# Kernel tuning notes

Hardware: AMD Instinct MI355X
Metric: run time of the kernel (lower is better)

The kernel has to match this reference:

```python
import jax, jax.numpy as jnp
import numpy as np

B, L, D, H = 8, 2048, 1024, 1024
BASE_LR, BASE_WD = 0.01, 0.9


def setup_inputs() -> dict:
    key = jax.random.key(0)
    ks = jax.random.split(key, 8)
    s = 1.0 / np.sqrt(D)
    return {
        "x": jax.random.normal(ks[0], (B, L, D), jnp.float32),
        "hidden": jax.random.normal(ks[1], (B, D, H), jnp.float32),
        "log_base_lr": jnp.array([np.log(BASE_LR)], jnp.float32),
        "w_lr": jax.random.normal(ks[2], (D, 1), jnp.float32) * s,
        "b_lr": jnp.zeros((1,), jnp.float32),
        "log_base_wd": jnp.array([np.log(BASE_WD)], jnp.float32),
        "w_wd": jax.random.normal(ks[3], (D, 1), jnp.float32) * s,
        "b_wd": jnp.zeros((1,), jnp.float32),
        "w_q": jax.random.normal(ks[4], (D, H), jnp.float32) * s,
        "b_q": jnp.zeros((H,), jnp.float32),
        "w_k": jax.random.normal(ks[5], (D, H), jnp.float32) * s,
        "b_k": jnp.zeros((H,), jnp.float32),
        "w_v": jax.random.normal(ks[6], (D, D), jnp.float32) * s,
        "b_v": jnp.zeros((D,), jnp.float32),
    }


def reference(x, hidden, log_base_lr, w_lr, b_lr, log_base_wd, w_wd, b_wd,
              w_q, b_q, w_k, b_k, w_v, b_v):
    batch, length, dim = x.shape
    W_prev = hidden  # [b, d, h]
    query = x @ w_q + b_q                     # [b, l, h]
    key = x @ w_k + b_k                       # [b, l, h]
    value = x @ w_v + b_v                     # [b, l, d]
    lr = jnp.exp(log_base_lr) * jax.nn.sigmoid((x @ w_lr + b_lr)[..., 0])  # [b, l]
    # log(1 - base_wd * sigmoid(.)) via log1p for stability; same math.
    log_wd = jnp.log1p(-jnp.exp(log_base_wd) * jax.nn.sigmoid((x @ w_wd + b_wd)[..., 0]))  # [b, l]
    wd_cross = jnp.exp(jnp.cumsum(log_wd, axis=1))  # [b, l]
    # inner-chunk decay: entry [b, m, l] = exp(sum_{j=m+1..l} log_wd[b, j]) for l >= m
    tri = jnp.triu(jnp.broadcast_to(log_wd[:, None, :], (batch, length, length)), k=1)
    wd_inner = jnp.triu(jnp.exp(jnp.cumsum(tri, axis=2)))  # [b, l, l]
    kq = jnp.einsum('bld,bmd->blm', key, query)            # [b, l, m]
    mask_kq = kq * wd_inner
    WpK_V = jnp.einsum('bdh,blh->bld', W_prev, key) - value  # [b, l, d]
    y_inner = -jnp.einsum('bld,bl,blm->bmd', WpK_V, lr, mask_kq)
    y_cross = jnp.einsum('bdh,blh,bl->bld', W_prev, query, wd_cross)
    y = y_inner + y_cross
    W_next_inner = -jnp.einsum('bld,bl,blh->bdh', WpK_V, lr * wd_inner[:, :, -1], key)
    W_next_cross = W_prev * wd_cross[:, -1][:, None, None]
    W_next = W_next_inner + W_next_cross
    return y, W_next
```

## Files before the change

kernel.cpp:

```cpp
#include <hip/hip_runtime.h>
#include <stdint.h>

#define BB 8
#define LL 2048
#define DD 1024
#define HH 1024
#define BL (BB*LL)

typedef __attribute__((ext_vector_type(8))) short short8;
typedef __attribute__((ext_vector_type(4))) float f32x4;

__device__ __forceinline__ unsigned short f2bf(float f) {
  unsigned int x = __float_as_uint(f);
  unsigned int r = (x + 0x7fffu + ((x >> 16) & 1u)) >> 16;
  return (unsigned short)r;
}
__device__ __forceinline__ float bf2f(unsigned short u) {
  return __uint_as_float(((unsigned int)u) << 16);
}

__device__ __forceinline__ void stage16(const unsigned short* g, unsigned short* l) {
  __builtin_amdgcn_global_load_lds((const __attribute__((address_space(1))) void*)g,
                                   (__attribute__((address_space(3))) void*)l,
                                   16, 0, 0);
}

template<int MI>
struct __align__(16) SmemT {
  unsigned short a[2][MI*2048];
  unsigned short b[2][16384];
};

template<int MI>
__device__ __forceinline__ void acc_initT(f32x4 (&acc)[MI][4]) {
#pragma unroll
  for (int i = 0; i < MI; ++i)
#pragma unroll
    for (int j = 0; j < 4; ++j)
      acc[i][j] = (f32x4){0.f, 0.f, 0.f, 0.f};
}

#define SCB __builtin_amdgcn_sched_barrier(0)
#define LGKM0 do { asm volatile("s_waitcnt lgkmcnt(0)" ::: "memory"); SCB; } while (0)

template<int MI, class FA, class FB>
__device__ __forceinline__ void gemm10_core(FA srcA, FB srcB, int NK,
                                            SmemT<MI>* sm, f32x4 (&acc)[MI][4]) {
  const int lane = threadIdx.x & 63;
  const int wave = threadIdx.x >> 6;
  const int srow = lane >> 3;
  const int scol = ((lane & 7) ^ srow) * 8;
  const int fk = (lane >> 4) * 8;
  const int fr = lane & 15;
  const int fx = fr & 7;
  const int mwr = (wave >> 2) * (MI * 16);
  const int nwr = (wave & 3) * 64;
  const int cA0 = (MI == 8) ? ((wave < 4) ? 2 * wave : 2 * wave + 8) : 2 * wave;
  const int cA1 = cA0 + 8;
  const int cB0 = (wave >> 1) * 8 + 2 * (wave & 1);
  const int cB1 = cB0 + 4;
  const int kc0 = (((fk >> 3) ^ fx) << 3);
  const int kc1 = ((((32 + fk) >> 3) ^ fx) << 3);

  auto SA2 = [&](int p, int kt, int c) {
    stage16(srcA(c * 8 + srow, kt) + scol, &sm->a[p][c * 512]);
    stage16(srcA(c * 8 + 8 + srow, kt) + scol, &sm->a[p][(c + 1) * 512]);
  };
  auto SB2 = [&](int p, int kt, int c) {
    stage16(srcB(c * 8 + srow, kt) + scol, &sm->b[p][c * 512]);
    stage16(srcB(c * 8 + 8 + srow, kt) + scol, &sm->b[p][(c + 1) * 512]);
  };

  short8 af[4], bfv[4][2];
  auto LDB = [&](int p) {
#pragma unroll
    for (int j = 0; j < 4; ++j) {
      bfv[j][0] = *(const short8*)&sm->b[p][(nwr + j * 16 + fr) * 64 + kc0];
      bfv[j][1] = *(const short8*)&sm->b[p][(nwr + j * 16 + fr) * 64 + kc1];
    }
  };
  auto LDA4 = [&](int p, int iho, int kc) {
#pragma unroll
    for (int i = 0; i < 4; ++i)
      af[i] = *(const short8*)&sm->a[p][(mwr + iho + i * 16 + fr) * 64 + kc];
  };
  auto MMk = [&](int accb, int kk) {
#pragma unroll
    for (int i = 0; i < 4; ++i)
#pragma unroll
      for (int j = 0; j < 4; ++j)
        acc[accb + i][j] = __builtin_amdgcn_mfma_f32_16x16x32_bf16(
            af[i], bfv[j][kk], acc[accb + i][j], 0, 0, 0);
  };

  SA2(0, 0, cA0);
  if constexpr (MI == 8) SA2(0, 0, cA1);
  SB2(0, 0, cB0); SB2(0, 0, cB1);
  if (NK > 1) {
    SB2(1, 1, cB0); SB2(1, 1, cB1);
    asm volatile("s_waitcnt vmcnt(4)" ::: "memory");
  } else {
    asm volatile("s_waitcnt vmcnt(0)" ::: "memory");
  }
  SCB; __builtin_amdgcn_s_barrier(); SCB;

  for (int t = 0; t < NK; ++t) {
    const int p = t & 1, po = p ^ 1;
    const bool s1 = (t + 1 < NK), s2 = (t + 2 < NK);
    if (s1) { SA2(po, t + 1, cA0); if constexpr (MI == 8) SA2(po, t + 1, cA1); }
    LDB(p);
    LDA4(p, 0, kc0);
    LGKM0;
    __builtin_amdgcn_s_setprio(1); MMk(0, 0); __builtin_amdgcn_s_setprio(0);
    if constexpr (MI == 8) {
      LDA4(p, 0, kc1);
      LGKM0;
      __builtin_amdgcn_s_setprio(1); MMk(0, 1); __builtin_amdgcn_s_setprio(0);
      SCB; __builtin_amdgcn_s_barrier(); SCB;
      if (s2) { SB2(p, t + 2, cB0); SB2(p, t + 2, cB1); }
      LDA4(p, 64, kc0);
      LGKM0;
      __builtin_amdgcn_s_setprio(1); MMk(4, 0); __builtin_amdgcn_s_setprio(0);
      LDA4(p, 64, kc1);
      LGKM0;
      __builtin_amdgcn_s_setprio(1); MMk(4, 1); __builtin_amdgcn_s_setprio(0);
    } else {
      SCB; __builtin_amdgcn_s_barrier(); SCB;
      if (s2) { SB2(p, t + 2, cB0); SB2(p, t + 2, cB1); }
      LDA4(p, 0, kc1);
      LGKM0;
      __builtin_amdgcn_s_setprio(1); MMk(0, 1); __builtin_amdgcn_s_setprio(0);
    }
    SCB;
    if (s2)      { asm volatile("s_waitcnt vmcnt(4)" ::: "memory"); }
    else if (s1) { asm volatile("s_waitcnt vmcnt(0)" ::: "memory"); }
    SCB; __builtin_amdgcn_s_barrier(); SCB;
  }
}

template<int MI, typename F>
__device__ __forceinline__ void epiT(const f32x4 (&acc)[MI][4], F body) {
  const int lane = threadIdx.x & 63;
  const int wave = threadIdx.x >> 6;
  const int mwr = (wave >> 2) * (MI * 16), nwr = (wave & 3) * 64;
#pragma unroll
  for (int i = 0; i < MI; ++i)
#pragma unroll
    for (int j = 0; j < 4; ++j)
#pragma unroll
      for (int jj = 0; jj < 4; ++jj)
        body(mwr + i * 16 + ((lane >> 4) << 2) + jj,
             nwr + j * 16 + (lane & 15), acc[i][j][jj]);
}


__global__ void k_prep_x(const float* __restrict__ x, const float* __restrict__ wlr,
                         const float* __restrict__ wwd, unsigned short* __restrict__ xb,
                         float* __restrict__ lrlog, float* __restrict__ wdlog) {
  const int wave = threadIdx.x >> 6, lane = threadIdx.x & 63;
  const int row = blockIdx.x * 4 + wave;
  const float* xr = x + (size_t)row * DD;
  float s1 = 0.f, s2 = 0.f;
#pragma unroll
  for (int ch = 0; ch < 4; ++ch) {
    const int col = ch * 256 + lane * 4;
    float4 v = *(const float4*)(xr + col);
    float4 a = *(const float4*)(wlr + col);
    float4 b = *(const float4*)(wwd + col);
    s1 += v.x*a.x + v.y*a.y + v.z*a.z + v.w*a.w;
    s2 += v.x*b.x + v.y*b.y + v.z*b.z + v.w*b.w;
    uint2 u;
    u.x = (unsigned)f2bf(v.x) | ((unsigned)f2bf(v.y) << 16);
    u.y = (unsigned)f2bf(v.z) | ((unsigned)f2bf(v.w) << 16);
    *(uint2*)(xb + (size_t)row * DD + col) = u;
  }
#pragma unroll
  for (int off = 32; off > 0; off >>= 1) {
    s1 += __shfl_down(s1, off);
    s2 += __shfl_down(s2, off);
  }
  if (lane == 0) { lrlog[row] = s1; wdlog[row] = s2; }
}

__global__ void k_prep_w(const float* __restrict__ wq, const float* __restrict__ wk,
                         const float* __restrict__ wv, unsigned short* __restrict__ wqt,
                         unsigned short* __restrict__ wkt, unsigned short* __restrict__ wvtn,
                         unsigned short* __restrict__ wkr) {
  const int idx = blockIdx.x * 256 + threadIdx.x;
  if (blockIdx.z == 3) { wkr[idx] = f2bf(wk[idx]); return; }
  const int k = idx >> 10, n = idx & 1023;
  const float* src = (blockIdx.z == 0) ? wq : (blockIdx.z == 1) ? wk : wv;
  unsigned short* dst = (blockIdx.z == 0) ? wqt : (blockIdx.z == 1) ? wkt : wvtn;
  float v = src[(size_t)k * 1024 + n];
  if (blockIdx.z == 2) v = -v;
  dst[(size_t)n * 1024 + k] = f2bf(v);
}

__global__ void k_prep_h(const float* __restrict__ hid, unsigned short* __restrict__ wpb) {
  const size_t i = ((size_t)blockIdx.x * 256 + threadIdx.x) * 4;
  float4 v = *(const float4*)(hid + i);
  uint2 u;
  u.x = (unsigned)f2bf(v.x) | ((unsigned)f2bf(v.y) << 16);
  u.y = (unsigned)f2bf(v.z) | ((unsigned)f2bf(v.w) << 16);
  *(uint2*)(wpb + i) = u;
}

__global__ void k_bias2(const unsigned short* __restrict__ wpb, const float* __restrict__ bk,
                        const float* __restrict__ bv, float* __restrict__ bias2) {
  const int wave = threadIdx.x >> 6, lane = threadIdx.x & 63;
  const int row = blockIdx.x * 4 + wave;
  const unsigned short* wr = wpb + (size_t)row * HH;
  float s = 0.f;
#pragma unroll
  for (int ch = 0; ch < 4; ++ch) {
    const int col = ch * 256 + lane * 4;
    float4 a = *(const float4*)(bk + col);
    ushort4 u = *(const ushort4*)(wr + col);
    s += a.x * bf2f(u.x) + a.y * bf2f(u.y) + a.z * bf2f(u.z) + a.w * bf2f(u.w);
  }
#pragma unroll
  for (int off = 32; off > 0; off >>= 1) s += __shfl_down(s, off);
  if (lane == 0) bias2[row] = s - bv[row & 1023];
}

__global__ void k_scan(const float* __restrict__ lrlog, const float* __restrict__ wdlog,
                       const float* __restrict__ lbl, const float* __restrict__ blr,
                       const float* __restrict__ lbw, const float* __restrict__ bwd,
                       float* __restrict__ lr, float* __restrict__ c,
                       float* __restrict__ s, float* __restrict__ ecl) {
  const int b = blockIdx.x, t = threadIdx.x;
  __shared__ float sums[256];
  const float elr = expf(lbl[0]);
  const float ewd = expf(lbw[0]);
  const float blr0 = blr[0], bwd0 = bwd[0];
  float lw[8];
  const float* wb = wdlog + (size_t)b * LL + t * 8;
  float tot = 0.f;
#pragma unroll
  for (int i = 0; i < 8; ++i) {
    float z = wb[i] + bwd0;
    float sig = 1.f / (1.f + expf(-z));
    tot += log1pf(-ewd * sig);
    lw[i] = tot;
  }
  sums[t] = tot;
  __syncthreads();
  for (int off = 1; off < 256; off <<= 1) {
    float v = (t >= off) ? sums[t - off] : 0.f;
    __syncthreads();
    sums[t] += v;
    __syncthreads();
  }
  const float prev = (t > 0) ? sums[t - 1] : 0.f;
  const float ctot = sums[255];
  const float* lb = lrlog + (size_t)b * LL + t * 8;
#pragma unroll
  for (int i = 0; i < 8; ++i) {
    const int idx = b * LL + t * 8 + i;
    const float ci = prev + lw[i];
    c[idx] = ci;
    float zl = lb[i] + blr0;
    float lri = elr / (1.f + expf(-zl));
    lr[idx] = lri;
    s[idx] = lri * expf(ctot - ci);
  }
  if (t == 0) ecl[b] = expf(ctot);
}


__global__ __launch_bounds__(512, 2) void k10_gemm_m2(const unsigned short* __restrict__ wpb,
    const unsigned short* __restrict__ wkr, const unsigned short* __restrict__ wvtn,
    unsigned short* __restrict__ w2t) {
  __shared__ SmemT<4> sm;
  const int b = blockIdx.x;
  const int mt = blockIdx.y & 7, nt = blockIdx.y >> 3;
  const int m0 = mt * 128, n0 = nt * 256;
  f32x4 acc[4][4]; acc_initT<4>(acc);
  gemm10_core<4>(
    [&](int r, int kt) { return wpb + (size_t)b * DD * HH + (size_t)(m0 + r) * HH + kt * 64; },
    [&](int r, int kt) { return wkr + (size_t)(n0 + r) * HH + kt * 64; },
    HH / 64, &sm, acc);
  epiT<4>(acc, [&](int rr, int cc, float av) {
    const size_t gi = (size_t)(m0 + rr) * DD + (n0 + cc);
    w2t[(size_t)b * DD * DD + gi] = f2bf(av + bf2f(wvtn[gi]));
  });
}

__global__ __launch_bounds__(512, 2) void k10_gemm_q(const unsigned short* __restrict__ xb,
    const unsigned short* __restrict__ wt, const float* __restrict__ bias,
    const float* __restrict__ c, unsigned short* __restrict__ outb,
    unsigned short* __restrict__ q2b) {
  __shared__ SmemT<8> sm;
  const int mt = blockIdx.x * 8 + (blockIdx.y & 7);
  const int nt = blockIdx.y >> 3;
  const int m0 = mt * 256, n0 = nt * 256;
  f32x4 acc[8][4]; acc_initT<8>(acc);
  gemm10_core<8>(
    [&](int r, int kt) { return xb + (size_t)(m0 + r) * DD + kt * 64; },
    [&](int r, int kt) { return wt + (size_t)(n0 + r) * DD + kt * 64; },
    DD / 64, &sm, acc);
  const int lane = threadIdx.x & 63, wave = threadIdx.x >> 6;
  const int mwr = (wave >> 2) * 128, nwr = (wave & 3) * 64;
  float er[8][4];
#pragma unroll
  for (int i = 0; i < 8; ++i)
#pragma unroll
    for (int jj = 0; jj < 4; ++jj)
      er[i][jj] = __expf(c[m0 + mwr + i * 16 + ((lane >> 4) << 2) + jj]);
#pragma unroll
  for (int i = 0; i < 8; ++i)
#pragma unroll
    for (int j = 0; j < 4; ++j)
#pragma unroll
      for (int jj = 0; jj < 4; ++jj) {
        const int row = m0 + mwr + i * 16 + ((lane >> 4) << 2) + jj;
        const int col = n0 + nwr + j * 16 + (lane & 15);
        const float v = acc[i][j][jj] + bias[col];
        outb[(size_t)row * HH + col] = f2bf(v);
        q2b[(size_t)row * HH + col] = f2bf(v * er[i][jj]);
      }
}

__global__ __launch_bounds__(512, 2) void k10_gemm_k(const unsigned short* __restrict__ xb,
    const unsigned short* __restrict__ wt, const float* __restrict__ bias,
    const float* __restrict__ s, unsigned short* __restrict__ kb,
    unsigned short* __restrict__ k2t) {
  __shared__ SmemT<8> sm;
  const int mt = blockIdx.x * 8 + (blockIdx.y & 7);
  const int nt = blockIdx.y >> 3;
  const int m0 = mt * 256, n0 = nt * 256;
  f32x4 acc[8][4]; acc_initT<8>(acc);
  gemm10_core<8>(
    [&](int r, int kt) { return xb + (size_t)(m0 + r) * DD + kt * 64; },
    [&](int r, int kt) { return wt + (size_t)(n0 + r) * DD + kt * 64; },
    DD / 64, &sm, acc);
  const int lane = threadIdx.x & 63, wave = threadIdx.x >> 6;
  const int mwr = (wave >> 2) * 128, nwr = (wave & 3) * 64;
#pragma unroll
  for (int i = 0; i < 8; ++i)
#pragma unroll
    for (int j = 0; j < 4; ++j) {
      const int col = n0 + nwr + j * 16 + (lane & 15);
      const float bias_c = bias[col];
      const int row0 = m0 + mwr + i * 16 + ((lane >> 4) << 2);
      const int b = row0 >> 11, ml0 = row0 & 2047;
      unsigned short tmp[4];
#pragma unroll
      for (int jj = 0; jj < 4; ++jj) {
        float v = acc[i][j][jj] + bias_c;
        kb[(size_t)(row0 + jj) * HH + col] = f2bf(v);
        tmp[jj] = f2bf(v * s[row0 + jj]);
      }
      uint2 u;
      u.x = (unsigned)tmp[0] | ((unsigned)tmp[1] << 16);
      u.y = (unsigned)tmp[2] | ((unsigned)tmp[3] << 16);
      *(uint2*)&k2t[((size_t)b * HH + col) * LL + ml0] = u;
    }
}

__global__ __launch_bounds__(512, 2) void k10_gemm_u(const unsigned short* __restrict__ xb,
    const unsigned short* __restrict__ w2t, const float* __restrict__ bias2,
    unsigned short* __restrict__ ut) {
  __shared__ SmemT<8> sm;
  const int b = blockIdx.x;
  const int mt = blockIdx.x * 8 + (blockIdx.y & 7);
  const int nt = blockIdx.y >> 3;
  const int m0 = mt * 256, n0 = nt * 256;
  f32x4 acc[8][4]; acc_initT<8>(acc);
  gemm10_core<8>(
    [&](int r, int kt) { return xb + (size_t)(m0 + r) * DD + kt * 64; },
    [&](int r, int kt) { return w2t + (size_t)b * DD * DD + (size_t)(n0 + r) * DD + kt * 64; },
    DD / 64, &sm, acc);
  const int lane = threadIdx.x & 63, wave = threadIdx.x >> 6;
  const int mwr = (wave >> 2) * 128, nwr = (wave & 3) * 64;
#pragma unroll
  for (int i = 0; i < 8; ++i)
#pragma unroll
    for (int j = 0; j < 4; ++j) {
      const int col = n0 + nwr + j * 16 + (lane & 15);
      const float b2c = bias2[b * DD + col];
      const int row0 = m0 + mwr + i * 16 + ((lane >> 4) << 2);
      const int ml0 = row0 & 2047;
      unsigned short tmp[4];
#pragma unroll
      for (int jj = 0; jj < 4; ++jj) tmp[jj] = f2bf(acc[i][j][jj] + b2c);
      uint2 u;
      u.x = (unsigned)tmp[0] | ((unsigned)tmp[1] << 16);
      u.y = (unsigned)tmp[2] | ((unsigned)tmp[3] << 16);
      *(uint2*)&ut[((size_t)b * DD + col) * LL + ml0] = u;
    }
}

__global__ __launch_bounds__(512, 2) void k10_gemm_p(const unsigned short* __restrict__ qb,
    const unsigned short* __restrict__ kb, const float* __restrict__ lr,
    const float* __restrict__ c, unsigned short* __restrict__ pb) {
  __shared__ SmemT<4> sm;
  const int b = blockIdx.x;
  const int t = blockIdx.y;
  int r = (int)((sqrtf(4.f * (float)t + 1.f) - 1.f) * 0.5f);
  while ((r + 1) * (r + 2) <= t) ++r;
  while (r * (r + 1) > t) --r;
  const int u = t - r * (r + 1);
  const int mt = 2 * r + (u > r ? 1 : 0);
  const int nt2 = (u > r) ? (u - r - 1) : u;
  const int base = b * LL;
  const int m0 = mt * 128, n0 = nt2 * 256;
  f32x4 acc[4][4]; acc_initT<4>(acc);
  gemm10_core<4>(
    [&](int rr, int kt) { return qb + (size_t)(base + m0 + rr) * HH + kt * 64; },
    [&](int rr, int kt) { return kb + (size_t)(base + n0 + rr) * HH + kt * 64; },
    HH / 64, &sm, acc);
  epiT<4>(acc, [&](int rr, int cc, float av) {
    const int m = m0 + rr, l = n0 + cc;
    float v = 0.f;
    if (l <= m) v = -av * lr[base + l] * __expf(c[base + m] - c[base + l]);
    pb[((size_t)base + m) * LL + l] = f2bf(v);
  });
}

__global__ __launch_bounds__(512, 2) void k10_gemm_y(const unsigned short* __restrict__ pb,
    const unsigned short* __restrict__ ut, const unsigned short* __restrict__ q2b,
    const unsigned short* __restrict__ wpb, float* __restrict__ out) {
  __shared__ SmemT<4> sm;
  const int b = blockIdx.x;
  const int sr = blockIdx.y & 7, nt = blockIdx.y >> 3;
  const int n0 = nt * 256;
  const unsigned short* pbB = pb + (size_t)b * LL * LL;
  const unsigned short* utB = ut + (size_t)b * DD * LL;
  const unsigned short* q2B = q2b + (size_t)b * LL * HH;
  const unsigned short* wpB = wpb + (size_t)b * DD * HH;
  f32x4 acc[4][4];
#pragma unroll
  for (int job = 0; job < 2; ++job) {
    const int mt = job ? (15 - sr) : sr;
    const int m0 = mt * 128;
    const int NK1 = (mt + 1) * 2;
    acc_initT<4>(acc);
    gemm10_core<4>(
      [&](int r, int kt) {
        return (kt < NK1) ? pbB + (size_t)(m0 + r) * LL + kt * 64
                          : q2B + (size_t)(m0 + r) * HH + (kt - NK1) * 64;
      },
      [&](int r, int kt) {
        return (kt < NK1) ? utB + (size_t)(n0 + r) * LL + kt * 64
                          : wpB + (size_t)(n0 + r) * HH + (kt - NK1) * 64;
      },
      NK1 + 16, &sm, acc);
    epiT<4>(acc, [&](int rr, int cc, float av) {
      out[((size_t)b * LL + m0 + rr) * DD + (n0 + cc)] = av;
    });
  }
}

__global__ __launch_bounds__(512, 2) void k10_gemm_wn(const unsigned short* __restrict__ ut,
    const unsigned short* __restrict__ k2t, const float* __restrict__ hid,
    const float* __restrict__ ecl, float* __restrict__ out2) {
  __shared__ SmemT<4> sm;
  const int b = blockIdx.x;
  const int mt = blockIdx.y & 7, nt = blockIdx.y >> 3;
  const int m0 = mt * 128, n0 = nt * 256;
  f32x4 acc[4][4]; acc_initT<4>(acc);
  gemm10_core<4>(
    [&](int r, int kt) { return ut + (size_t)b * DD * LL + (size_t)(m0 + r) * LL + kt * 64; },
    [&](int r, int kt) { return k2t + (size_t)b * HH * LL + (size_t)(n0 + r) * LL + kt * 64; },
    LL / 64, &sm, acc);
  const float eclb = ecl[b];
  epiT<4>(acc, [&](int rr, int cc, float av) {
    const size_t gi = ((size_t)b * DD + (m0 + rr)) * HH + (n0 + cc);
    out2[gi] = -av + eclb * hid[gi];
  });
}


extern "C" void kernel_launch(void* const* d_in, const int* in_sizes, int n_in,
                              void* d_out, int out_size, void* d_ws, size_t ws_size,
                              hipStream_t stream) {
  (void)in_sizes; (void)n_in; (void)out_size; (void)ws_size;
  const float* x   = (const float*)d_in[0];
  const float* hid = (const float*)d_in[1];
  const float* lbl = (const float*)d_in[2];
  const float* wlr = (const float*)d_in[3];
  const float* blr = (const float*)d_in[4];
  const float* lbw = (const float*)d_in[5];
  const float* wwd = (const float*)d_in[6];
  const float* bwd = (const float*)d_in[7];
  const float* wq  = (const float*)d_in[8];
  const float* bq  = (const float*)d_in[9];
  const float* wk  = (const float*)d_in[10];
  const float* bk  = (const float*)d_in[11];
  const float* wv  = (const float*)d_in[12];
  const float* bv  = (const float*)d_in[13];
  float* out = (float*)d_out;

  char* w = (char*)d_ws;
  constexpr size_t SZ_XB  = (size_t)BL * DD * 2;
  constexpr size_t SZ_QB  = (size_t)BL * HH * 2;
  constexpr size_t SZ_KB  = (size_t)BL * HH * 2;
  constexpr size_t SZ_K2T = (size_t)BB * HH * LL * 2;
  constexpr size_t SZ_UT  = (size_t)BB * DD * LL * 2;
  constexpr size_t SZ_PB  = (size_t)BB * LL * LL * 2;
  constexpr size_t SZ_WT  = (size_t)DD * HH * 2;
  constexpr size_t SZ_WPB = (size_t)BB * DD * HH * 2;
  constexpr size_t SZ_V16 = (size_t)BL * 4;

  size_t off = 0;
  unsigned short* xb   = (unsigned short*)(w + off); off += SZ_XB;
  unsigned short* qb   = (unsigned short*)(w + off); off += SZ_QB;
  unsigned short* kb   = (unsigned short*)(w + off); off += SZ_KB;
  unsigned short* k2t  = (unsigned short*)(w + off); off += SZ_K2T;
  unsigned short* ut   = (unsigned short*)(w + off); off += SZ_UT;
  unsigned short* pb   = (unsigned short*)(w + off); off += SZ_PB;
  unsigned short* wqt  = (unsigned short*)(w + off); off += SZ_WT;
  unsigned short* wkt  = (unsigned short*)(w + off); off += SZ_WT;
  unsigned short* wvtn = (unsigned short*)(w + off); off += SZ_WT;
  unsigned short* wpb  = (unsigned short*)(w + off); off += SZ_WPB;
  float* lrlog = (float*)(w + off); off += SZ_V16;
  float* wdlog = (float*)(w + off); off += SZ_V16;
  float* lr    = (float*)(w + off); off += SZ_V16;
  float* c     = (float*)(w + off); off += SZ_V16;
  float* s     = (float*)(w + off); off += SZ_V16;
  float* ecl   = (float*)(w + off); off += 256;
  float* bias2 = (float*)(w + off); off += (size_t)BB * DD * 4;

  unsigned short* w2t = pb;
  unsigned short* wkr = pb + (size_t)BB * DD * DD;

  unsigned short* q2b = (unsigned short*)(out + (size_t)BL * DD);
  float* out2 = out + (size_t)BL * DD;

  k_prep_x<<<dim3(BL / 4), 256, 0, stream>>>(x, wlr, wwd, xb, lrlog, wdlog);
  k_prep_w<<<dim3(4096, 1, 4), 256, 0, stream>>>(wq, wk, wv, wqt, wkt, wvtn, wkr);
  k_prep_h<<<dim3((unsigned)((size_t)BB * DD * HH / 1024)), 256, 0, stream>>>(hid, wpb);
  k_scan<<<dim3(BB), 256, 0, stream>>>(lrlog, wdlog, lbl, blr, lbw, bwd, lr, c, s, ecl);
  k_bias2<<<dim3(BB * DD / 4), 256, 0, stream>>>(wpb, bk, bv, bias2);

  k10_gemm_m2<<<dim3(8, 32), 512, 0, stream>>>(wpb, wkr, wvtn, w2t);
  k10_gemm_q<<<dim3(8, 32), 512, 0, stream>>>(xb, wqt, bq, c, qb, q2b);
  k10_gemm_k<<<dim3(8, 32), 512, 0, stream>>>(xb, wkt, bk, s, kb, k2t);
  k10_gemm_u<<<dim3(8, 32), 512, 0, stream>>>(xb, w2t, bias2, ut);
  k10_gemm_p<<<dim3(8, 72), 512, 0, stream>>>(qb, kb, lr, c, pb);
  k10_gemm_y<<<dim3(8, 32), 512, 0, stream>>>(pb, ut, q2b, wpb, out);
  k10_gemm_wn<<<dim3(8, 32), 512, 0, stream>>>(ut, k2t, hid, ecl, out2);
}
```

Baseline: 581.2 us.

## Split MI=8 GEMM k-step into barrier-separated phases and retile y GEMM to 256 rows

In the 256-row GEMM core, each k-step is split into four phases. Each phase loads its own B and A fragments and issues part of the next tile's global-to-LDS staging, then runs a workgroup barrier before its MFMAs, so memory traffic spreads across the step and waves stay in lockstep. Separately, the y GEMM drops its 128-row, two-job triangular balancing in favour of one 256-row tile per block using the MI=8 core. That gives more reuse per tile but risks load imbalance, because row tiles now have different causal K lengths and the pairing no longer evens them out. The extra barriers per k-step may also add stalls.

```diff
diff --git a/kernel.cpp b/kernel.cpp
--- a/kernel.cpp
+++ b/kernel.cpp
@@ -44,7 +44,7 @@
 #define LGKM0 do { asm volatile("s_waitcnt lgkmcnt(0)" ::: "memory"); SCB; } while (0)
 
 template<int MI, class FA, class FB>
-__device__ __forceinline__ void gemm10_core(FA srcA, FB srcB, int NK,
+__device__ __forceinline__ void gemm11_core(FA srcA, FB srcB, int NK,
                                             SmemT<MI>* sm, f32x4 (&acc)[MI][4]) {
   const int lane = threadIdx.x & 63;
   const int wave = threadIdx.x >> 6;
@@ -79,6 +79,11 @@
       bfv[j][1] = *(const short8*)&sm->b[p][(nwr + j * 16 + fr) * 64 + kc1];
     }
   };
+  auto LDBk = [&](int p, int kk, int kc) {
+#pragma unroll
+    for (int j = 0; j < 4; ++j)
+      bfv[j][kk] = *(const short8*)&sm->b[p][(nwr + j * 16 + fr) * 64 + kc];
+  };
   auto LDA4 = [&](int p, int iho, int kc) {
 #pragma unroll
     for (int i = 0; i < 4; ++i)
@@ -107,34 +112,48 @@
   for (int t = 0; t < NK; ++t) {
     const int p = t & 1, po = p ^ 1;
     const bool s1 = (t + 1 < NK), s2 = (t + 2 < NK);
-    if (s1) { SA2(po, t + 1, cA0); if constexpr (MI == 8) SA2(po, t + 1, cA1); }
-    LDB(p);
-    LDA4(p, 0, kc0);
-    LGKM0;
-    __builtin_amdgcn_s_setprio(1); MMk(0, 0); __builtin_amdgcn_s_setprio(0);
     if constexpr (MI == 8) {
+      LDBk(p, 0, kc0);
+      LDA4(p, 0, kc0);
+      if (s1) SA2(po, t + 1, cA0);
+      SCB; __builtin_amdgcn_s_barrier(); LGKM0;
+      __builtin_amdgcn_s_setprio(1); MMk(0, 0); __builtin_amdgcn_s_setprio(0);
+      SCB; __builtin_amdgcn_s_barrier(); SCB;
+      LDBk(p, 1, kc1);
       LDA4(p, 0, kc1);
-      LGKM0;
+      if (s1) SA2(po, t + 1, cA1);
+      SCB; __builtin_amdgcn_s_barrier(); LGKM0;
       __builtin_amdgcn_s_setprio(1); MMk(0, 1); __builtin_amdgcn_s_setprio(0);
       SCB; __builtin_amdgcn_s_barrier(); SCB;
-      if (s2) { SB2(p, t + 2, cB0); SB2(p, t + 2, cB1); }
       LDA4(p, 64, kc0);
+      if (s2) SB2(p, t + 2, cB0);
+      SCB; __builtin_amdgcn_s_barrier(); LGKM0;
+      __builtin_amdgcn_s_setprio(1); MMk(4, 0); __builtin_amdgcn_s_setprio(0);
+      SCB; __builtin_amdgcn_s_barrier(); SCB;
+      LDA4(p, 64, kc1);
+      if (s2) SB2(p, t + 2, cB1);
+      SCB; __builtin_amdgcn_s_barrier(); LGKM0;
+      __builtin_amdgcn_s_setprio(1); MMk(4, 1); __builtin_amdgcn_s_setprio(0);
+      SCB;
+      if (s2)      { asm volatile("s_waitcnt vmcnt(4)" ::: "memory"); }
+      else if (s1) { asm volatile("s_waitcnt vmcnt(0)" ::: "memory"); }
+      SCB; __builtin_amdgcn_s_barrier(); SCB;
+    } else {
+      if (s1) SA2(po, t + 1, cA0);
+      LDB(p);
+      LDA4(p, 0, kc0);
       LGKM0;
-      __builtin_amdgcn_s_setprio(1); MMk(4, 0); __builtin_amdgcn_s_setprio(0);
-      LDA4(p, 64, kc1);
-      LGKM0;
-      __builtin_amdgcn_s_setprio(1); MMk(4, 1); __builtin_amdgcn_s_setprio(0);
-    } else {
+      __builtin_amdgcn_s_setprio(1); MMk(0, 0); __builtin_amdgcn_s_setprio(0);
       SCB; __builtin_amdgcn_s_barrier(); SCB;
       if (s2) { SB2(p, t + 2, cB0); SB2(p, t + 2, cB1); }
       LDA4(p, 0, kc1);
       LGKM0;
       __builtin_amdgcn_s_setprio(1); MMk(0, 1); __builtin_amdgcn_s_setprio(0);
+      SCB;
+      if (s2)      { asm volatile("s_waitcnt vmcnt(4)" ::: "memory"); }
+      else if (s1) { asm volatile("s_waitcnt vmcnt(0)" ::: "memory"); }
+      SCB; __builtin_amdgcn_s_barrier(); SCB;
     }
-    SCB;
-    if (s2)      { asm volatile("s_waitcnt vmcnt(4)" ::: "memory"); }
-    else if (s1) { asm volatile("s_waitcnt vmcnt(0)" ::: "memory"); }
-    SCB; __builtin_amdgcn_s_barrier(); SCB;
   }
 }
 
@@ -268,7 +287,7 @@
 }
 
 
-__global__ __launch_bounds__(512, 2) void k10_gemm_m2(const unsigned short* __restrict__ wpb,
+__global__ __launch_bounds__(512, 2) void k11_gemm_m2(const unsigned short* __restrict__ wpb,
     const unsigned short* __restrict__ wkr, const unsigned short* __restrict__ wvtn,
     unsigned short* __restrict__ w2t) {
   __shared__ SmemT<4> sm;
@@ -276,7 +295,7 @@
   const int mt = blockIdx.y & 7, nt = blockIdx.y >> 3;
   const int m0 = mt * 128, n0 = nt * 256;
   f32x4 acc[4][4]; acc_initT<4>(acc);
-  gemm10_core<4>(
+  gemm11_core<4>(
     [&](int r, int kt) { return wpb + (size_t)b * DD * HH + (size_t)(m0 + r) * HH + kt * 64; },
     [&](int r, int kt) { return wkr + (size_t)(n0 + r) * HH + kt * 64; },
     HH / 64, &sm, acc);
@@ -286,7 +305,7 @@
   });
 }
 
-__global__ __launch_bounds__(512, 2) void k10_gemm_q(const unsigned short* __restrict__ xb,
+__global__ __launch_bounds__(512, 2) void k11_gemm_q(const unsigned short* __restrict__ xb,
     const unsigned short* __restrict__ wt, const float* __restrict__ bias,
     const float* __restrict__ c, unsigned short* __restrict__ outb,
     unsigned short* __restrict__ q2b) {
@@ -295,7 +314,7 @@
   const int nt = blockIdx.y >> 3;
   const int m0 = mt * 256, n0 = nt * 256;
   f32x4 acc[8][4]; acc_initT<8>(acc);
-  gemm10_core<8>(
+  gemm11_core<8>(
     [&](int r, int kt) { return xb + (size_t)(m0 + r) * DD + kt * 64; },
     [&](int r, int kt) { return wt + (size_t)(n0 + r) * DD + kt * 64; },
     DD / 64, &sm, acc);
@@ -321,7 +340,7 @@
       }
 }
 
-__global__ __launch_bounds__(512, 2) void k10_gemm_k(const unsigned short* __restrict__ xb,
+__global__ __launch_bounds__(512, 2) void k11_gemm_k(const unsigned short* __restrict__ xb,
     const unsigned short* __restrict__ wt, const float* __restrict__ bias,
     const float* __restrict__ s, unsigned short* __restrict__ kb,
     unsigned short* __restrict__ k2t) {
@@ -330,7 +349,7 @@
   const int nt = blockIdx.y >> 3;
   const int m0 = mt * 256, n0 = nt * 256;
   f32x4 acc[8][4]; acc_initT<8>(acc);
-  gemm10_core<8>(
+  gemm11_core<8>(
     [&](int r, int kt) { return xb + (size_t)(m0 + r) * DD + kt * 64; },
     [&](int r, int kt) { return wt + (size_t)(n0 + r) * DD + kt * 64; },
     DD / 64, &sm, acc);
@@ -358,7 +377,7 @@
     }
 }
 
-__global__ __launch_bounds__(512, 2) void k10_gemm_u(const unsigned short* __restrict__ xb,
+__global__ __launch_bounds__(512, 2) void k11_gemm_u(const unsigned short* __restrict__ xb,
     const unsigned short* __restrict__ w2t, const float* __restrict__ bias2,
     unsigned short* __restrict__ ut) {
   __shared__ SmemT<8> sm;
@@ -367,7 +386,7 @@
   const int nt = blockIdx.y >> 3;
   const int m0 = mt * 256, n0 = nt * 256;
   f32x4 acc[8][4]; acc_initT<8>(acc);
-  gemm10_core<8>(
+  gemm11_core<8>(
     [&](int r, int kt) { return xb + (size_t)(m0 + r) * DD + kt * 64; },
     [&](int r, int kt) { return w2t + (size_t)b * DD * DD + (size_t)(n0 + r) * DD + kt * 64; },
     DD / 64, &sm, acc);
@@ -391,7 +410,7 @@
     }
 }
 
-__global__ __launch_bounds__(512, 2) void k10_gemm_p(const unsigned short* __restrict__ qb,
+__global__ __launch_bounds__(512, 2) void k11_gemm_p(const unsigned short* __restrict__ qb,
     const unsigned short* __restrict__ kb, const float* __restrict__ lr,
     const float* __restrict__ c, unsigned short* __restrict__ pb) {
   __shared__ SmemT<4> sm;
@@ -406,7 +425,7 @@
   const int base = b * LL;
   const int m0 = mt * 128, n0 = nt2 * 256;
   f32x4 acc[4][4]; acc_initT<4>(acc);
-  gemm10_core<4>(
+  gemm11_core<4>(
     [&](int rr, int kt) { return qb + (size_t)(base + m0 + rr) * HH + kt * 64; },
     [&](int rr, int kt) { return kb + (size_t)(base + n0 + rr) * HH + kt * 64; },
     HH / 64, &sm, acc);
@@ -418,41 +437,32 @@
   });
 }
 
-__global__ __launch_bounds__(512, 2) void k10_gemm_y(const unsigned short* __restrict__ pb,
+__global__ __launch_bounds__(512, 2) void k11_gemm_y(const unsigned short* __restrict__ pb,
     const unsigned short* __restrict__ ut, const unsigned short* __restrict__ q2b,
     const unsigned short* __restrict__ wpb, float* __restrict__ out) {
-  __shared__ SmemT<4> sm;
+  __shared__ SmemT<8> sm;
   const int b = blockIdx.x;
-  const int sr = blockIdx.y & 7, nt = blockIdx.y >> 3;
-  const int n0 = nt * 256;
-  const unsigned short* pbB = pb + (size_t)b * LL * LL;
-  const unsigned short* utB = ut + (size_t)b * DD * LL;
-  const unsigned short* q2B = q2b + (size_t)b * LL * HH;
-  const unsigned short* wpB = wpb + (size_t)b * DD * HH;
-  f32x4 acc[4][4];
-#pragma unroll
-  for (int job = 0; job < 2; ++job) {
-    const int mt = job ? (15 - sr) : sr;
-    const int m0 = mt * 128;
-    const int NK1 = (mt + 1) * 2;
-    acc_initT<4>(acc);
-    gemm10_core<4>(
-      [&](int r, int kt) {
-        return (kt < NK1) ? pbB + (size_t)(m0 + r) * LL + kt * 64
-                          : q2B + (size_t)(m0 + r) * HH + (kt - NK1) * 64;
-      },
-      [&](int r, int kt) {
-        return (kt < NK1) ? utB + (size_t)(n0 + r) * LL + kt * 64
-                          : wpB + (size_t)(n0 + r) * HH + (kt - NK1) * 64;
-      },
-      NK1 + 16, &sm, acc);
-    epiT<4>(acc, [&](int rr, int cc, float av) {
-      out[((size_t)b * LL + m0 + rr) * DD + (n0 + cc)] = av;
-    });
-  }
-}
-
-__global__ __launch_bounds__(512, 2) void k10_gemm_wn(const unsigned short* __restrict__ ut,
+  const int mt = blockIdx.y & 7;
+  const int nt = blockIdx.y >> 3;
+  const int m0 = mt * 256, n0 = nt * 256;
+  const int NK1 = (mt + 1) * 4;
+  f32x4 acc[8][4]; acc_initT<8>(acc);
+  gemm11_core<8>(
+    [&](int r, int kt) {
+      return (kt < NK1) ? pb + (size_t)b * LL * LL + (size_t)(m0 + r) * LL + kt * 64
+                        : q2b + ((size_t)b * LL + m0 + r) * HH + (kt - NK1) * 64;
+    },
+    [&](int r, int kt) {
+      return (kt < NK1) ? ut + (size_t)b * DD * LL + (size_t)(n0 + r) * LL + kt * 64
+                        : wpb + (size_t)b * DD * HH + (size_t)(n0 + r) * HH + (kt - NK1) * 64;
+    },
+    NK1 + 16, &sm, acc);
+  epiT<8>(acc, [&](int rr, int cc, float av) {
+    out[((size_t)b * LL + m0 + rr) * DD + (n0 + cc)] = av;
+  });
+}
+
+__global__ __launch_bounds__(512, 2) void k11_gemm_wn(const unsigned short* __restrict__ ut,
     const unsigned short* __restrict__ k2t, const float* __restrict__ hid,
     const float* __restrict__ ecl, float* __restrict__ out2) {
   __shared__ SmemT<4> sm;
@@ -460,7 +470,7 @@
   const int mt = blockIdx.y & 7, nt = blockIdx.y >> 3;
   const int m0 = mt * 128, n0 = nt * 256;
   f32x4 acc[4][4]; acc_initT<4>(acc);
-  gemm10_core<4>(
+  gemm11_core<4>(
     [&](int r, int kt) { return ut + (size_t)b * DD * LL + (size_t)(m0 + r) * LL + kt * 64; },
     [&](int r, int kt) { return k2t + (size_t)b * HH * LL + (size_t)(n0 + r) * LL + kt * 64; },
     LL / 64, &sm, acc);
@@ -534,11 +544,11 @@
   k_scan<<<dim3(BB), 256, 0, stream>>>(lrlog, wdlog, lbl, blr, lbw, bwd, lr, c, s, ecl);
   k_bias2<<<dim3(BB * DD / 4), 256, 0, stream>>>(wpb, bk, bv, bias2);
 
-  k10_gemm_m2<<<dim3(8, 32), 512, 0, stream>>>(wpb, wkr, wvtn, w2t);
-  k10_gemm_q<<<dim3(8, 32), 512, 0, stream>>>(xb, wqt, bq, c, qb, q2b);
-  k10_gemm_k<<<dim3(8, 32), 512, 0, stream>>>(xb, wkt, bk, s, kb, k2t);
-  k10_gemm_u<<<dim3(8, 32), 512, 0, stream>>>(xb, w2t, bias2, ut);
-  k10_gemm_p<<<dim3(8, 72), 512, 0, stream>>>(qb, kb, lr, c, pb);
-  k10_gemm_y<<<dim3(8, 32), 512, 0, stream>>>(pb, ut, q2b, wpb, out);
-  k10_gemm_wn<<<dim3(8, 32), 512, 0, stream>>>(ut, k2t, hid, ecl, out2);
-}
+  k11_gemm_m2<<<dim3(8, 32), 512, 0, stream>>>(wpb, wkr, wvtn, w2t);
+  k11_gemm_q<<<dim3(8, 32), 512, 0, stream>>>(xb, wqt, bq, c, qb, q2b);
+  k11_gemm_k<<<dim3(8, 32), 512, 0, stream>>>(xb, wkt, bk, s, kb, k2t);
+  k11_gemm_u<<<dim3(8, 32), 512, 0, stream>>>(xb, w2t, bias2, ut);
+  k11_gemm_p<<<dim3(8, 72), 512, 0, stream>>>(qb, kb, lr, c, pb);
+  k11_gemm_y<<<dim3(8, 32), 512, 0, stream>>>(pb, ut, q2b, wpb, out);
+  k11_gemm_wn<<<dim3(8, 32), 512, 0, stream>>>(ut, k2t, hid, ecl, out2);
+}
```

New measurement: 580.6 us. No clear change (-0.1%).
